# Kernel optimization log

Hardware: AMD Instinct MI355X
Metric: run time of the kernel (lower is better)

## Reference

```python
import jax, jax.numpy as jnp
import numpy as np

B, N, M, D = 8, 1024, 2048, 1024


def setup_inputs() -> dict:
    key = jax.random.key(0)
    k1, k2, k3 = jax.random.split(key, 3)
    text_features = jax.random.normal(k1, (B, N, D), dtype=jnp.float32)
    audio_features = jax.random.normal(k2, (B, M, D), dtype=jnp.float32)
    sigma = jnp.ones((1,), dtype=jnp.float32)  # learnable bandwidth, initial_sigma=1.0
    # audio lengths in [M//4, M) so no softmax row is fully masked
    audio_lengths = jnp.maximum(
        jax.random.randint(k3, (B,), 0, M), M // 4
    ).astype(jnp.int32)
    return {
        "text_features": text_features,
        "audio_features": audio_features,
        "sigma": sigma,
        "audio_lengths": audio_lengths,
    }


def reference(text_features, audio_features, sigma, audio_lengths):
    b, n, d = text_features.shape
    m = audio_features.shape[1]
    s = jnp.abs(sigma[0]) + 1e-8

    # QK^T / sqrt(d)  -> (B, N, M)
    scores = jnp.einsum("bnd,bmd->bnm", text_features, audio_features) / jnp.sqrt(
        jnp.float32(d)
    )

    # Gaussian relative positional bias: -|i/N - j/M|^2 / (2 sigma^2)
    text_pos = jnp.arange(n, dtype=jnp.float32) / n    # (N,)
    audio_pos = jnp.arange(m, dtype=jnp.float32) / m   # (M,)
    d_rel = jnp.abs(text_pos[:, None] - audio_pos[None, :])  # (N, M)
    scores = scores - d_rel**2 / (2.0 * s * s)

    # mask padded audio positions per batch element
    valid = jnp.arange(m)[None, :] < audio_lengths[:, None]  # (B, M) bool
    scores = jnp.where(valid[:, None, :], scores, -jnp.inf)

    attention_weights = jax.nn.softmax(scores, axis=-1)  # (B, N, M)
    enhanced = jnp.einsum("bnm,bmd->bnd", attention_weights, audio_features)
    return enhanced, attention_weights
```

## Files before the change

### kernel.cpp

```cpp
#include <hip/hip_runtime.h>
#include <hip/hip_bf16.h>

#define BB 8
#define NN 1024
#define MM 2048
#define DD 1024

typedef __attribute__((ext_vector_type(8))) __bf16 bfrag8;
typedef __attribute__((ext_vector_type(4))) float ffrag4;

__device__ __forceinline__ unsigned short f2bf(float f) {
  union { float f; unsigned u; } x; x.f = f;
  unsigned r = x.u + 0x7FFFu + ((x.u >> 16) & 1u);
  return (unsigned short)(r >> 16);
}

__device__ __forceinline__ void gload_lds16(const unsigned short* g, unsigned short* l) {
  __builtin_amdgcn_global_load_lds(
      (const __attribute__((address_space(1))) void*)g,
      (__attribute__((address_space(3))) void*)l, 16, 0, 0);
}

#define SCHED0() __builtin_amdgcn_sched_barrier(0)
#define MFMA16x16x32 __builtin_amdgcn_mfma_f32_16x16x32_bf16

__device__ __forceinline__ void stage_half(const unsigned short* gbase, int ldk,
                                           unsigned short* ldst,
                                           int w, int r0, int slog) {
  const unsigned short* g = gbase + (size_t)(w * 8 + r0) * ldk + slog;
  gload_lds16(g, ldst + w * 512);
  gload_lds16(g + (size_t)64 * ldk, ldst + 4096 + w * 512);
}

#define TSTR 68
__global__ __launch_bounds__(256) void ta_prep(
    const float* __restrict__ Q, const float* __restrict__ V,
    unsigned short* __restrict__ Qbf,
    unsigned short* __restrict__ Kbf, unsigned short* __restrict__ VT,
    float* __restrict__ sums)
{
  __shared__ unsigned short Tls[64 * TSTR];
  const int bid = blockIdx.x;
  const int t = threadIdx.x;

  if (bid < 4096) {
    int tt = bid * 256 + t;
    const float4* src = reinterpret_cast<const float4*>(Q) + tt * 2;
    float4 a = src[0], b = src[1];
    ushort4 lo = { f2bf(a.x), f2bf(a.y), f2bf(a.z), f2bf(a.w) };
    ushort4 hi = { f2bf(b.x), f2bf(b.y), f2bf(b.z), f2bf(b.w) };
    ushort4* dst = reinterpret_cast<ushort4*>(Qbf) + tt * 2;
    dst[0] = lo; dst[1] = hi;
  } else if (bid < 8192) {
    const int id = bid - 4096;
    const int dt = id & 15;
    const int mt = (id >> 4) & 31;
    const int b  = id >> 9;

    const float* Vb = V + (size_t)b * MM * DD + (size_t)(mt * 64) * DD + dt * 64;
#pragma unroll
    for (int it = 0; it < 4; ++it) {
      int slot = t + 256 * it;
      int row  = slot >> 4;
      int c4   = slot & 15;
      float4 a = *reinterpret_cast<const float4*>(Vb + (size_t)row * DD + c4 * 4);
      ushort4 h = { f2bf(a.x), f2bf(a.y), f2bf(a.z), f2bf(a.w) };
      *reinterpret_cast<ushort4*>(&Tls[row * TSTR + c4 * 4]) = h;
    }
    __syncthreads();

    unsigned short* Kb = Kbf + (size_t)b * MM * DD + (size_t)(mt * 64) * DD + dt * 64;
    unsigned short* Vt = VT  + (size_t)b * DD * MM + (size_t)(dt * 64) * MM + mt * 64;
#pragma unroll
    for (int it = 0; it < 4; ++it) {
      int slot = t + 256 * it;
      int row  = slot >> 4;
      int c4   = slot & 15;
      *reinterpret_cast<ushort4*>(Kb + (size_t)row * DD + c4 * 4) =
          *reinterpret_cast<const ushort4*>(&Tls[row * TSTR + c4 * 4]);
      ushort4 tv = { Tls[(c4 * 4 + 0) * TSTR + row],
                     Tls[(c4 * 4 + 1) * TSTR + row],
                     Tls[(c4 * 4 + 2) * TSTR + row],
                     Tls[(c4 * 4 + 3) * TSTR + row] };
      *reinterpret_cast<ushort4*>(Vt + (size_t)row * MM + c4 * 4) = tv;
    }
  } else {
    int tt = (bid - 8192) * 256 + t;
    sums[tt] = 0.0f;
  }
}

__global__ void ta_zero(float* __restrict__ sums) {
  int t = blockIdx.x * 256 + threadIdx.x;
  if (t < BB * NN) sums[t] = 0.0f;
}

__global__ __launch_bounds__(512, 2) void ta_gemm1x(
    const unsigned short* __restrict__ Q,
    const unsigned short* __restrict__ K,
    const float* __restrict__ sigma,
    const int* __restrict__ lens,
    unsigned short* __restrict__ Ebf,
    float* __restrict__ rowsum)
{
  const int lin = blockIdx.x + 8 * (blockIdx.y + 4 * blockIdx.z);
  const int wid = (lin & 7) * 32 + (lin >> 3);
  const int bj = wid & 7, bi = (wid >> 3) & 3, b = wid >> 5;

  const int t = threadIdx.x;
  const int lane = t & 63, w = t >> 6;
  const int wr = w >> 2, wc = w & 3;
  __shared__ unsigned short S[65536];

  const unsigned short* Qb = Q + (size_t)b * NN * DD + (size_t)(bi * 256) * DD;
  const unsigned short* Kb = K + (size_t)b * MM * DD + (size_t)(bj * 256) * DD;

  const int r  = lane & 15, qd = lane >> 4;
  const int r0 = (lane >> 3) & 7;
  const int slog = ((lane & 7) ^ r0) << 3;
  const int cs0 = ((qd)     ^ (r & 7)) << 3;
  const int cs1 = ((4 + qd) ^ (r & 7)) << 3;

  ffrag4 acc[8][4] = {};

  {
    unsigned short* T0 = &S[0];
    stage_half(Qb,                        DD, T0,          w, r0, slog);
    stage_half(Qb + (size_t)128 * DD,     DD, T0 + 8192,   w, r0, slog);
    stage_half(Kb,                        DD, T0 + 16384,  w, r0, slog);
    stage_half(Kb + (size_t)128 * DD,     DD, T0 + 24576,  w, r0, slog);
    unsigned short* T1 = &S[32768];
    stage_half(Qb + 64,                    DD, T1,          w, r0, slog);
    stage_half(Qb + (size_t)128 * DD + 64, DD, T1 + 8192,   w, r0, slog);
    stage_half(Kb + 64,                    DD, T1 + 16384,  w, r0, slog);
    stage_half(Kb + (size_t)128 * DD + 64, DD, T1 + 24576,  w, r0, slog);
    asm volatile("s_waitcnt vmcnt(8)" ::: "memory");
    __builtin_amdgcn_s_barrier();
  }

#pragma unroll 2
  for (int kt = 0; kt < 16; ++kt) {
    const int p = kt & 1;
    unsigned short* Ab = &S[p * 32768 + wr * 8192];
    unsigned short* Bb = &S[p * 32768 + 16384 + (wc >> 1) * 8192];
    const int brb = (wc & 1) * 64;
    bfrag8 af[4][2], bf0[2][2], bf1[2][2];

#pragma unroll
    for (int mi = 0; mi < 4; ++mi) {
      const unsigned short* a = &Ab[(mi * 16 + r) * 64];
      af[mi][0] = *reinterpret_cast<const bfrag8*>(a + cs0);
      af[mi][1] = *reinterpret_cast<const bfrag8*>(a + cs1);
    }
#pragma unroll
    for (int jj = 0; jj < 2; ++jj) {
      const unsigned short* bp = &Bb[(brb + jj * 16 + r) * 64];
      bf0[jj][0] = *reinterpret_cast<const bfrag8*>(bp + cs0);
      bf0[jj][1] = *reinterpret_cast<const bfrag8*>(bp + cs1);
    }
    asm volatile("s_waitcnt lgkmcnt(0)" ::: "memory");
    SCHED0(); __builtin_amdgcn_s_setprio(1);
#pragma unroll
    for (int mi = 0; mi < 4; ++mi)
#pragma unroll
      for (int jj = 0; jj < 2; ++jj) {
        acc[mi][jj] = MFMA16x16x32(af[mi][0], bf0[jj][0], acc[mi][jj], 0, 0, 0);
        acc[mi][jj] = MFMA16x16x32(af[mi][1], bf0[jj][1], acc[mi][jj], 0, 0, 0);
      }
    __builtin_amdgcn_s_setprio(0); SCHED0();

#pragma unroll
    for (int jj = 0; jj < 2; ++jj) {
      const unsigned short* bp = &Bb[(brb + (2 + jj) * 16 + r) * 64];
      bf1[jj][0] = *reinterpret_cast<const bfrag8*>(bp + cs0);
      bf1[jj][1] = *reinterpret_cast<const bfrag8*>(bp + cs1);
    }
    asm volatile("s_waitcnt lgkmcnt(0)" ::: "memory");
    SCHED0(); __builtin_amdgcn_s_barrier();
    __builtin_amdgcn_s_setprio(1);
#pragma unroll
    for (int mi = 0; mi < 4; ++mi)
#pragma unroll
      for (int jj = 0; jj < 2; ++jj) {
        acc[mi][2 + jj] = MFMA16x16x32(af[mi][0], bf1[jj][0], acc[mi][2 + jj], 0, 0, 0);
        acc[mi][2 + jj] = MFMA16x16x32(af[mi][1], bf1[jj][1], acc[mi][2 + jj], 0, 0, 0);
      }
    __builtin_amdgcn_s_setprio(0); SCHED0();

#pragma unroll
    for (int mi = 0; mi < 4; ++mi) {
      const unsigned short* a = &Ab[((mi + 4) * 16 + r) * 64];
      af[mi][0] = *reinterpret_cast<const bfrag8*>(a + cs0);
      af[mi][1] = *reinterpret_cast<const bfrag8*>(a + cs1);
    }
    if (kt + 2 < 16) {
      unsigned short* Dst = &S[p * 32768 + 16384];
      stage_half(Kb + (kt + 2) * 64,                    DD, Dst,        w, r0, slog);
      stage_half(Kb + (size_t)128 * DD + (kt + 2) * 64, DD, Dst + 8192, w, r0, slog);
    }
    asm volatile("s_waitcnt lgkmcnt(0)" ::: "memory");
    SCHED0(); __builtin_amdgcn_s_barrier();
    __builtin_amdgcn_s_setprio(1);
#pragma unroll
    for (int mi = 0; mi < 4; ++mi)
#pragma unroll
      for (int jj = 0; jj < 2; ++jj) {
        acc[4 + mi][2 + jj] = MFMA16x16x32(af[mi][0], bf1[jj][0], acc[4 + mi][2 + jj], 0, 0, 0);
        acc[4 + mi][2 + jj] = MFMA16x16x32(af[mi][1], bf1[jj][1], acc[4 + mi][2 + jj], 0, 0, 0);
      }
    __builtin_amdgcn_s_setprio(0); SCHED0();

    if (kt + 2 < 16) {
      unsigned short* Dst = &S[p * 32768];
      stage_half(Qb + (kt + 2) * 64,                    DD, Dst,        w, r0, slog);
      stage_half(Qb + (size_t)128 * DD + (kt + 2) * 64, DD, Dst + 8192, w, r0, slog);
    }
    SCHED0(); __builtin_amdgcn_s_setprio(1);
#pragma unroll
    for (int mi = 0; mi < 4; ++mi)
#pragma unroll
      for (int jj = 0; jj < 2; ++jj) {
        acc[4 + mi][jj] = MFMA16x16x32(af[mi][0], bf0[jj][0], acc[4 + mi][jj], 0, 0, 0);
        acc[4 + mi][jj] = MFMA16x16x32(af[mi][1], bf0[jj][1], acc[4 + mi][jj], 0, 0, 0);
      }
    __builtin_amdgcn_s_setprio(0); SCHED0();
    if (kt + 2 < 16)      { asm volatile("s_waitcnt vmcnt(8)" ::: "memory"); }
    else if (kt + 1 < 16) { asm volatile("s_waitcnt vmcnt(0)" ::: "memory"); }
    __builtin_amdgcn_s_barrier();
  }

  const float sg = fabsf(sigma[0]) + 1e-8f;
  const float inv2s2 = 1.0f / (2.0f * sg * sg);
  const int len = lens[b];
  unsigned short* Erow = Ebf + (size_t)b * NN * MM;
  float* sums = rowsum + (size_t)b * NN;
  const int ibase = bi * 256 + wr * 128;
  const int jbase = bj * 256 + wc * 64;
#pragma unroll
  for (int mi = 0; mi < 8; ++mi) {
#pragma unroll
    for (int v = 0; v < 4; ++v) {
      int i = ibase + mi * 16 + qd * 4 + v;
      float psum = 0.0f;
#pragma unroll
      for (int nj = 0; nj < 4; ++nj) {
        int j = jbase + nj * 16 + r;
        float e = 0.0f;
        if (j < len) {
          float dr = (float)i * (1.0f / (float)NN) - (float)j * (1.0f / (float)MM);
          float sc = acc[mi][nj][v] * 0.03125f - dr * dr * inv2s2;
          e = __expf(fminf(sc, 30.0f));
        }
        psum += e;
        Erow[(size_t)i * MM + j] = f2bf(e);
      }
      psum += __shfl_xor(psum, 1);
      psum += __shfl_xor(psum, 2);
      psum += __shfl_xor(psum, 4);
      psum += __shfl_xor(psum, 8);
      if (r == 0) atomicAdd(&sums[i], psum);
    }
  }
}

__global__ __launch_bounds__(512, 2) void ta_gemm2x(
    const unsigned short* __restrict__ E,
    const unsigned short* __restrict__ VT,
    const float* __restrict__ rowsum,
    float* __restrict__ O,
    float* __restrict__ attn)
{
  const int lin = blockIdx.x + 4 * (blockIdx.y + 8 * blockIdx.z);
  const int wid = (lin & 7) * 32 + (lin >> 3);
  const int bd = wid & 3, bi = (wid >> 2) & 7, b = wid >> 5;

  const int t = threadIdx.x;
  const int lane = t & 63, w = t >> 6;
  const int wr = w >> 2, wc = w & 3;
  __shared__ unsigned short S[49152];

  const unsigned short* Eb = E  + (size_t)b * NN * MM + (size_t)(bi * 128) * MM;
  const unsigned short* Vb = VT + (size_t)b * DD * MM + (size_t)(bd * 256) * MM;

  const int r  = lane & 15, qd = lane >> 4;
  const int r0 = (lane >> 3) & 7;
  const int slog = ((lane & 7) ^ r0) << 3;
  const int cs0 = ((qd)     ^ (r & 7)) << 3;
  const int cs1 = ((4 + qd) ^ (r & 7)) << 3;

  ffrag4 acc[4][4] = {};

  const float* rsB = rowsum + (size_t)b * NN;
  const float* rsT = rsB + bi * 128;
  float* attnB = attn + ((size_t)b * NN + bi * 128) * MM + bd * 512;
  const unsigned short* Eslice = Eb + bd * 512;
  uint4 ax = {0, 0, 0, 0};
  float ainv = 0.0f;
  int arow = 0, acol = 0;

  {
    stage_half(Eb,                        MM, &S[0],     w, r0, slog);
    stage_half(Vb,                        MM, &S[8192],  w, r0, slog);
    stage_half(Vb + (size_t)128 * MM,     MM, &S[16384], w, r0, slog);
    stage_half(Eb + 64,                    MM, &S[24576],         w, r0, slog);
    stage_half(Vb + 64,                    MM, &S[24576 + 8192],  w, r0, slog);
    stage_half(Vb + (size_t)128 * MM + 64, MM, &S[24576 + 16384], w, r0, slog);
    asm volatile("s_waitcnt vmcnt(6)" ::: "memory");
    __builtin_amdgcn_s_barrier();
  }

#pragma unroll 2
  for (int kt = 0; kt < 32; ++kt) {
    const int p = kt & 1;
    unsigned short* Ab = &S[p * 24576];
    unsigned short* Bb = &S[p * 24576 + 8192 + (wc >> 1) * 8192];
    const int arb = wr * 64;
    const int brb = (wc & 1) * 64;
    bfrag8 af[4][2], bf[4][2];

#pragma unroll
    for (int mi = 0; mi < 4; ++mi) {
      const unsigned short* a = &Ab[(arb + mi * 16 + r) * 64];
      af[mi][0] = *reinterpret_cast<const bfrag8*>(a + cs0);
      af[mi][1] = *reinterpret_cast<const bfrag8*>(a + cs1);
    }
#pragma unroll
    for (int nj = 0; nj < 4; ++nj) {
      const unsigned short* bp = &Bb[(brb + nj * 16 + r) * 64];
      bf[nj][0] = *reinterpret_cast<const bfrag8*>(bp + cs0);
      bf[nj][1] = *reinterpret_cast<const bfrag8*>(bp + cs1);
    }

    if ((kt & 1) == 0) {
      int it = kt >> 1;
      int c = t + it * 512;
      arow = c >> 6;
      acol = (c & 63) * 8;
      ax = *reinterpret_cast<const uint4*>(Eslice + (size_t)arow * MM + acol);
      ainv = 1.0f / fmaxf(rsT[arow], 1e-30f);
    } else {
      unsigned u[4] = { ax.x, ax.y, ax.z, ax.w };
      float o[8];
#pragma unroll
      for (int k2 = 0; k2 < 4; ++k2) {
        union { unsigned u; float f; } lo, hi;
        lo.u = u[k2] << 16; hi.u = u[k2] & 0xFFFF0000u;
        o[2 * k2]     = lo.f * ainv;
        o[2 * k2 + 1] = hi.f * ainv;
      }
      float4* dst = reinterpret_cast<float4*>(attnB + (size_t)arow * MM + acol);
      float4 f0 = { o[0], o[1], o[2], o[3] };
      float4 f1 = { o[4], o[5], o[6], o[7] };
      dst[0] = f0; dst[1] = f1;
    }

    asm volatile("s_waitcnt lgkmcnt(0)" ::: "memory");
    SCHED0(); __builtin_amdgcn_s_barrier();
    __builtin_amdgcn_s_setprio(1);
#pragma unroll
    for (int mi = 0; mi < 2; ++mi)
#pragma unroll
      for (int nj = 0; nj < 4; ++nj) {
        acc[mi][nj] = MFMA16x16x32(af[mi][0], bf[nj][0], acc[mi][nj], 0, 0, 0);
        acc[mi][nj] = MFMA16x16x32(af[mi][1], bf[nj][1], acc[mi][nj], 0, 0, 0);
      }
    __builtin_amdgcn_s_setprio(0); SCHED0();

    if (kt + 2 < 32) {
      unsigned short* Dst = &S[p * 24576];
      stage_half(Eb + (kt + 2) * 64,                    MM, Dst,         w, r0, slog);
      stage_half(Vb + (kt + 2) * 64,                    MM, Dst + 8192,  w, r0, slog);
      stage_half(Vb + (size_t)128 * MM + (kt + 2) * 64, MM, Dst + 16384, w, r0, slog);
    }

    SCHED0(); __builtin_amdgcn_s_setprio(1);
#pragma unroll
    for (int mi = 2; mi < 4; ++mi)
#pragma unroll
      for (int nj = 0; nj < 4; ++nj) {
        acc[mi][nj] = MFMA16x16x32(af[mi][0], bf[nj][0], acc[mi][nj], 0, 0, 0);
        acc[mi][nj] = MFMA16x16x32(af[mi][1], bf[nj][1], acc[mi][nj], 0, 0, 0);
      }
    __builtin_amdgcn_s_setprio(0); SCHED0();

    if (kt + 2 < 32)      { asm volatile("s_waitcnt vmcnt(6)" ::: "memory"); }
    else if (kt + 1 < 32) { asm volatile("s_waitcnt vmcnt(0)" ::: "memory"); }
    __builtin_amdgcn_s_barrier();
  }

  float* Ob = O + (size_t)b * NN * DD;
  const int ibase = bi * 128 + wr * 64;
  const int dbase = bd * 256 + wc * 64;
#pragma unroll
  for (int mi = 0; mi < 4; ++mi) {
#pragma unroll
    for (int v = 0; v < 4; ++v) {
      int i = ibase + mi * 16 + qd * 4 + v;
      float inv = 1.0f / fmaxf(rsB[i], 1e-30f);
#pragma unroll
      for (int nj = 0; nj < 4; ++nj) {
        int d = dbase + nj * 16 + r;
        Ob[(size_t)i * DD + d] = acc[mi][nj][v] * inv;
      }
    }
  }
}

#define LDA 40
__global__ __launch_bounds__(256) void tb_gemm1e(
    const float* __restrict__ Q, const float* __restrict__ K,
    const float* __restrict__ sigma, const int* __restrict__ lens,
    float* __restrict__ attn, float* __restrict__ rowsum)
{
  const int bj = blockIdx.x, bi = blockIdx.y, b = blockIdx.z;
  const int t = threadIdx.x;
  const int lane = t & 63;
  const int w = t >> 6;
  const int wi = w >> 1, wj = w & 1;
  __shared__ unsigned short Als[128 * LDA];
  __shared__ unsigned short Bls[128 * LDA];
  const float* Qb = Q + (size_t)b * NN * DD + (size_t)(bi * 128) * DD;
  const float* Kb = K + (size_t)b * MM * DD + (size_t)(bj * 128) * DD;
  ffrag4 acc[4][4] = {};
  const int r = lane & 15;
  const int koff = (lane >> 4) * 8;
  for (int k0 = 0; k0 < DD; k0 += 32) {
#pragma unroll
    for (int it = 0; it < 4; ++it) {
      int slot = t + 256 * it;
      int row = slot >> 3, c4 = slot & 7;
      float4 qa = *reinterpret_cast<const float4*>(Qb + (size_t)row * DD + k0 + c4 * 4);
      float4 ka = *reinterpret_cast<const float4*>(Kb + (size_t)row * DD + k0 + c4 * 4);
      ushort4 qh = { f2bf(qa.x), f2bf(qa.y), f2bf(qa.z), f2bf(qa.w) };
      ushort4 kh = { f2bf(ka.x), f2bf(ka.y), f2bf(ka.z), f2bf(ka.w) };
      *reinterpret_cast<ushort4*>(&Als[row * LDA + c4 * 4]) = qh;
      *reinterpret_cast<ushort4*>(&Bls[row * LDA + c4 * 4]) = kh;
    }
    __syncthreads();
    bfrag8 af[4], bf[4];
#pragma unroll
    for (int ti = 0; ti < 4; ++ti)
      af[ti] = *reinterpret_cast<const bfrag8*>(&Als[(wi * 64 + ti * 16 + r) * LDA + koff]);
#pragma unroll
    for (int tj = 0; tj < 4; ++tj)
      bf[tj] = *reinterpret_cast<const bfrag8*>(&Bls[(wj * 64 + tj * 16 + r) * LDA + koff]);
#pragma unroll
    for (int ti = 0; ti < 4; ++ti)
#pragma unroll
      for (int tj = 0; tj < 4; ++tj)
        acc[ti][tj] = MFMA16x16x32(af[ti], bf[tj], acc[ti][tj], 0, 0, 0);
    __syncthreads();
  }
  const float s = fabsf(sigma[0]) + 1e-8f;
  const float inv2s2 = 1.0f / (2.0f * s * s);
  const int len = lens[b];
  float* Prow = attn + (size_t)b * NN * MM;
  float* sums = rowsum + (size_t)b * NN;
  const int ibase = bi * 128 + wi * 64;
  const int jbase = bj * 128 + wj * 64;
  const int quad = lane >> 4;
#pragma unroll
  for (int ti = 0; ti < 4; ++ti) {
#pragma unroll
    for (int v = 0; v < 4; ++v) {
      int i = ibase + ti * 16 + quad * 4 + v;
      float psum = 0.0f;
#pragma unroll
      for (int tj = 0; tj < 4; ++tj) {
        int j = jbase + tj * 16 + r;
        float e = 0.0f;
        if (j < len) {
          float dr = (float)i * (1.0f / (float)NN) - (float)j * (1.0f / (float)MM);
          float sc = acc[ti][tj][v] * 0.03125f - dr * dr * inv2s2;
          e = __expf(fminf(sc, 30.0f));
        }
        psum += e;
        Prow[(size_t)i * MM + j] = e;
      }
      psum += __shfl_xor(psum, 1);
      psum += __shfl_xor(psum, 2);
      psum += __shfl_xor(psum, 4);
      psum += __shfl_xor(psum, 8);
      if (r == 0) atomicAdd(&sums[i], psum);
    }
  }
}

__global__ __launch_bounds__(256) void tb_norm(float* __restrict__ attn,
                                               const float* __restrict__ sums) {
  int t = blockIdx.x * 256 + threadIdx.x;
  int row = t >> 9;
  const float inv = 1.0f / fmaxf(sums[row], 1e-30f);
  float4* p = reinterpret_cast<float4*>(attn) + t;
  float4 x = *p;
  x.x *= inv; x.y *= inv; x.z *= inv; x.w *= inv;
  *p = x;
}

__global__ __launch_bounds__(256) void tb_gemm2(
    const float* __restrict__ P, const float* __restrict__ V, float* __restrict__ O)
{
  const int bd = blockIdx.x, bi = blockIdx.y, b = blockIdx.z;
  const int t = threadIdx.x;
  const int lane = t & 63;
  const int w = t >> 6;
  const int wi = w >> 1, wj = w & 1;
  __shared__ unsigned short Pls[128 * LDA];
  __shared__ unsigned short Vls[128 * LDA];
  const float* Pb = P + (size_t)b * NN * MM + (size_t)(bi * 128) * MM;
  const float* Vb = V + (size_t)b * MM * DD + bd * 128;
  ffrag4 acc[4][4] = {};
  const int r = lane & 15;
  const int koff = (lane >> 4) * 8;
  const int vd = t & 127;
  const int vmb = (t >> 7) * 16;
  for (int k0 = 0; k0 < MM; k0 += 32) {
#pragma unroll
    for (int it = 0; it < 4; ++it) {
      int slot = t + 256 * it;
      int row = slot >> 3, c4 = slot & 7;
      float4 pa = *reinterpret_cast<const float4*>(Pb + (size_t)row * MM + k0 + c4 * 4);
      ushort4 ph = { f2bf(pa.x), f2bf(pa.y), f2bf(pa.z), f2bf(pa.w) };
      *reinterpret_cast<ushort4*>(&Pls[row * LDA + c4 * 4]) = ph;
    }
    union { unsigned short h[16]; uint4 q[2]; } hv;
#pragma unroll
    for (int i = 0; i < 16; ++i)
      hv.h[i] = f2bf(Vb[(size_t)(k0 + vmb + i) * DD + vd]);
    *reinterpret_cast<uint4*>(&Vls[vd * LDA + vmb]) = hv.q[0];
    *reinterpret_cast<uint4*>(&Vls[vd * LDA + vmb + 8]) = hv.q[1];
    __syncthreads();
    bfrag8 af[4], bf[4];
#pragma unroll
    for (int ti = 0; ti < 4; ++ti)
      af[ti] = *reinterpret_cast<const bfrag8*>(&Pls[(wi * 64 + ti * 16 + r) * LDA + koff]);
#pragma unroll
    for (int tj = 0; tj < 4; ++tj)
      bf[tj] = *reinterpret_cast<const bfrag8*>(&Vls[(wj * 64 + tj * 16 + r) * LDA + koff]);
#pragma unroll
    for (int ti = 0; ti < 4; ++ti)
#pragma unroll
      for (int tj = 0; tj < 4; ++tj)
        acc[ti][tj] = MFMA16x16x32(af[ti], bf[tj], acc[ti][tj], 0, 0, 0);
    __syncthreads();
  }
  float* Ob = O + (size_t)b * NN * DD;
  const int ibase = bi * 128 + wi * 64;
  const int dbase = bd * 128 + wj * 64;
#pragma unroll
  for (int ti = 0; ti < 4; ++ti) {
#pragma unroll
    for (int tj = 0; tj < 4; ++tj) {
      int d = dbase + tj * 16 + r;
#pragma unroll
      for (int v = 0; v < 4; ++v) {
        int i = ibase + ti * 16 + (lane >> 4) * 4 + v;
        Ob[(size_t)i * DD + d] = acc[ti][tj][v];
      }
    }
  }
}

extern "C" void kernel_launch(void* const* d_in, const int* in_sizes, int n_in,
                              void* d_out, int out_size, void* d_ws, size_t ws_size,
                              hipStream_t stream) {
  const float* text  = (const float*)d_in[0];
  const float* audio = (const float*)d_in[1];
  const float* sigma = (const float*)d_in[2];
  const int*   lens  = (const int*)d_in[3];

  float* out = (float*)d_out;
  float* enhanced = out;
  float* attn = out + (size_t)BB * NN * DD;

  const size_t QBF  = (size_t)BB * NN * DD * 2;
  const size_t KBF  = (size_t)BB * MM * DD * 2;
  const size_t VTB  = (size_t)BB * DD * MM * 2;
  const size_t EBF  = (size_t)BB * NN * MM * 2;
  const size_t offQ = 65536;
  const size_t offK = offQ + QBF;
  const size_t offV = offK + KBF;
  const size_t offE = offV + VTB;
  const size_t need = offE + EBF;

  float* rowsum = (float*)d_ws;

  if (ws_size >= need) {
    unsigned short* Qbf = (unsigned short*)((char*)d_ws + offQ);
    unsigned short* Kbf = (unsigned short*)((char*)d_ws + offK);
    unsigned short* VT  = (unsigned short*)((char*)d_ws + offV);
    unsigned short* Ebf = (unsigned short*)((char*)d_ws + offE);

    ta_prep<<<dim3(8224), 256, 0, stream>>>(text, audio, Qbf, Kbf, VT, rowsum);
    ta_gemm1x<<<dim3(MM / 256, NN / 256, BB), 512, 0, stream>>>(Qbf, Kbf, sigma, lens, Ebf, rowsum);
    ta_gemm2x<<<dim3(DD / 256, NN / 128, BB), 512, 0, stream>>>(Ebf, VT, rowsum, enhanced, attn);
  } else {
    ta_zero<<<dim3((BB * NN + 255) / 256), 256, 0, stream>>>(rowsum);
    tb_gemm1e<<<dim3(MM / 128, NN / 128, BB), 256, 0, stream>>>(text, audio, sigma, lens, attn, rowsum);
    tb_norm<<<dim3(BB * NN * MM / 4 / 256), 256, 0, stream>>>(attn, rowsum);
    tb_gemm2<<<dim3(DD / 128, NN / 128, BB), 256, 0, stream>>>(attn, audio, enhanced);
  }
}
```

Measured before the change: 263.6 us.

## Stage exp tile through LDS for coalesced stores; emit attn from staged LDS tiles

In the first GEMM kernel, each wave now writes its bf16 exp tile into a padded LDS scratch region and then copies it out to global memory with 16-byte row-contiguous stores, replacing scattered 2-byte stores. In the second GEMM kernel, the normalized attention output is no longer built from separate global re-reads of E. It reads the E tile already staged in LDS for the matching column window and writes 16 floats per thread. This cuts uncoalesced stores and redundant global reads, at the cost of more LDS in gemm1 and some extra LDS traffic and wait points in gemm2.

```diff
diff --git a/kernel.cpp b/kernel.cpp
--- a/kernel.cpp
+++ b/kernel.cpp
@@ -110,7 +110,7 @@
   const int t = threadIdx.x;
   const int lane = t & 63, w = t >> 6;
   const int wr = w >> 2, wc = w & 3;
-  __shared__ unsigned short S[65536];
+  __shared__ unsigned short S[73728];
 
   const unsigned short* Qb = Q + (size_t)b * NN * DD + (size_t)(bi * 256) * DD;
   const unsigned short* Kb = K + (size_t)b * MM * DD + (size_t)(bj * 256) * DD;
@@ -236,11 +236,14 @@
   float* sums = rowsum + (size_t)b * NN;
   const int ibase = bi * 256 + wr * 128;
   const int jbase = bj * 256 + wc * 64;
+  unsigned short* W = &S[w * 9216];
+
 #pragma unroll
   for (int mi = 0; mi < 8; ++mi) {
 #pragma unroll
     for (int v = 0; v < 4; ++v) {
-      int i = ibase + mi * 16 + qd * 4 + v;
+      int lrow = mi * 16 + qd * 4 + v;
+      int i = ibase + lrow;
       float psum = 0.0f;
 #pragma unroll
       for (int nj = 0; nj < 4; ++nj) {
@@ -252,7 +255,7 @@
           e = __expf(fminf(sc, 30.0f));
         }
         psum += e;
-        Erow[(size_t)i * MM + j] = f2bf(e);
+        W[lrow * 72 + nj * 16 + r] = f2bf(e);
       }
       psum += __shfl_xor(psum, 1);
       psum += __shfl_xor(psum, 2);
@@ -260,6 +263,14 @@
       psum += __shfl_xor(psum, 8);
       if (r == 0) atomicAdd(&sums[i], psum);
     }
+  }
+  asm volatile("s_waitcnt lgkmcnt(0)" ::: "memory");
+  const int rrow = lane >> 3, c8 = lane & 7;
+#pragma unroll
+  for (int pp = 0; pp < 16; ++pp) {
+    int row = pp * 8 + rrow;
+    uint4 val = *reinterpret_cast<const uint4*>(&W[row * 72 + c8 * 8]);
+    *reinterpret_cast<uint4*>(Erow + (size_t)(ibase + row) * MM + jbase + c8 * 8) = val;
   }
 }
 
@@ -291,12 +302,12 @@
   ffrag4 acc[4][4] = {};
 
   const float* rsB = rowsum + (size_t)b * NN;
-  const float* rsT = rsB + bi * 128;
-  float* attnB = attn + ((size_t)b * NN + bi * 128) * MM + bd * 512;
-  const unsigned short* Eslice = Eb + bd * 512;
-  uint4 ax = {0, 0, 0, 0};
-  float ainv = 0.0f;
-  int arow = 0, acol = 0;
+  const int arow = t >> 2;
+  const int lcb  = (t & 3) * 2;
+  const int apc0 = (lcb)     ^ (arow & 7);
+  const int apc1 = (lcb + 1) ^ (arow & 7);
+  const float ainv = 1.0f / fmaxf(rsB[bi * 128 + arow], 1e-30f);
+  float* attnRowBase = attn + ((size_t)b * NN + bi * 128 + arow) * MM;
 
   {
     stage_half(Eb,                        MM, &S[0],     w, r0, slog);
@@ -317,6 +328,8 @@
     const int arb = wr * 64;
     const int brb = (wc & 1) * 64;
     bfrag8 af[4][2], bf[4][2];
+    const bool awin = ((kt >> 3) == bd);
+    uint4 av0, av1;
 
 #pragma unroll
     for (int mi = 0; mi < 4; ++mi) {
@@ -330,32 +343,34 @@
       bf[nj][0] = *reinterpret_cast<const bfrag8*>(bp + cs0);
       bf[nj][1] = *reinterpret_cast<const bfrag8*>(bp + cs1);
     }
-
-    if ((kt & 1) == 0) {
-      int it = kt >> 1;
-      int c = t + it * 512;
-      arow = c >> 6;
-      acol = (c & 63) * 8;
-      ax = *reinterpret_cast<const uint4*>(Eslice + (size_t)arow * MM + acol);
-      ainv = 1.0f / fmaxf(rsT[arow], 1e-30f);
-    } else {
-      unsigned u[4] = { ax.x, ax.y, ax.z, ax.w };
-      float o[8];
-#pragma unroll
-      for (int k2 = 0; k2 < 4; ++k2) {
+    if (awin) {
+      av0 = *reinterpret_cast<const uint4*>(&Ab[arow * 64 + apc0 * 8]);
+      av1 = *reinterpret_cast<const uint4*>(&Ab[arow * 64 + apc1 * 8]);
+    }
+
+    asm volatile("s_waitcnt lgkmcnt(0)" ::: "memory");
+    SCHED0(); __builtin_amdgcn_s_barrier();
+
+    if (awin) {
+      float* dst = attnRowBase + kt * 64 + lcb * 8;
+      unsigned u[8] = { av0.x, av0.y, av0.z, av0.w, av1.x, av1.y, av1.z, av1.w };
+      float o[16];
+#pragma unroll
+      for (int k2 = 0; k2 < 8; ++k2) {
         union { unsigned u; float f; } lo, hi;
         lo.u = u[k2] << 16; hi.u = u[k2] & 0xFFFF0000u;
         o[2 * k2]     = lo.f * ainv;
         o[2 * k2 + 1] = hi.f * ainv;
       }
-      float4* dst = reinterpret_cast<float4*>(attnB + (size_t)arow * MM + acol);
-      float4 f0 = { o[0], o[1], o[2], o[3] };
-      float4 f1 = { o[4], o[5], o[6], o[7] };
-      dst[0] = f0; dst[1] = f1;
-    }
-
-    asm volatile("s_waitcnt lgkmcnt(0)" ::: "memory");
-    SCHED0(); __builtin_amdgcn_s_barrier();
+      float4* d4 = reinterpret_cast<float4*>(dst);
+      float4 f0 = { o[0],  o[1],  o[2],  o[3]  };
+      float4 f1 = { o[4],  o[5],  o[6],  o[7]  };
+      float4 f2 = { o[8],  o[9],  o[10], o[11] };
+      float4 f3 = { o[12], o[13], o[14], o[15] };
+      d4[0] = f0; d4[1] = f1; d4[2] = f2; d4[3] = f3;
+    }
+    SCHED0();
+
     __builtin_amdgcn_s_setprio(1);
 #pragma unroll
     for (int mi = 0; mi < 2; ++mi)
```

Result: no change. 265.7 us (+0.8%).
